# Performance work log

Measured on AMD Instinct MI355X. Metric: run time of the kernel, lower is better.

Reference implementation:

```python
import jax, jax.numpy as jnp
from jax import lax
import numpy as np

L, B, D_IN, D_OUT, D_MLP = 64, 32, 512, 512, 128
WINDOWS = [1, 3]
FEATS = [256, 128]
C = sum(FEATS)  # 384
EPS = 1e-5


def _leaky(x):
    return jnp.where(x >= 0, x, 0.1 * x)


def setup_inputs() -> dict:
    key = jax.random.key(0)
    ks = jax.random.split(key, 16)
    s = lambda k, shp: (jax.random.normal(k, shp, jnp.float32) * 0.02)
    inp = {}
    inp["x"] = jax.random.normal(ks[0], (L, B, D_IN), jnp.float32)
    inp["xs_mask"] = jnp.ones((L, B), jnp.float32)
    # conv + batchnorm params per window
    inp["conv_w0"] = s(ks[1], (FEATS[0], 1, D_IN * WINDOWS[0]))
    inp["conv_b0"] = jnp.zeros((FEATS[0],), jnp.float32)
    inp["gamma0"] = jnp.ones((FEATS[0],), jnp.float32)
    inp["beta0"] = jnp.zeros((FEATS[0],), jnp.float32)
    inp["conv_w1"] = s(ks[2], (FEATS[1], 1, D_IN * WINDOWS[1]))
    inp["conv_b1"] = jnp.zeros((FEATS[1],), jnp.float32)
    inp["gamma1"] = jnp.ones((FEATS[1],), jnp.float32)
    inp["beta1"] = jnp.zeros((FEATS[1],), jnp.float32)
    inp["w0"] = s(ks[3], (2 * C, D_MLP)); inp["b0"] = jnp.zeros((D_MLP,), jnp.float32)
    inp["w1"] = s(ks[4], (D_MLP, D_MLP)); inp["b1"] = jnp.zeros((D_MLP,), jnp.float32)
    inp["w2"] = s(ks[5], (D_MLP, D_MLP)); inp["b2"] = jnp.zeros((D_MLP,), jnp.float32)
    inp["w3"] = s(ks[6], (D_MLP, D_MLP)); inp["b3"] = jnp.zeros((D_MLP,), jnp.float32)
    # output MLP: Linear(d_mlp->d_mlp), Linear(d_mlp->d_out)
    inp["w4"] = s(ks[7], (D_MLP, D_MLP)); inp["b4"] = jnp.zeros((D_MLP,), jnp.float32)
    inp["w5"] = s(ks[8], (D_MLP, D_OUT)); inp["b5"] = jnp.zeros((D_OUT,), jnp.float32)
    return inp


def reference(x, xs_mask, conv_w0, conv_b0, gamma0, beta0, conv_w1, conv_b1,
              gamma1, beta1, w0, b0, w1, b1, w2, b2, w3, b3, w4, b4, w5, b5):
    # x: (L, B, E)
    x = x * xs_mask[:, :, None]
    xf = jnp.transpose(x, (1, 0, 2)).reshape(B, 1, L * D_IN)  # (B, 1, L*E)

    # CNN front-end: Conv1d(stride=d_in) + BatchNorm1d (batch stats) + LeakyReLU
    feats = []
    for win, cw, cb, g, bt in [(WINDOWS[0], conv_w0, conv_b0, gamma0, beta0),
                               (WINDOWS[1], conv_w1, conv_b1, gamma1, beta1)]:
        pad = (win - 1) // 2 * D_IN
        y = lax.conv_general_dilated(xf, cw, window_strides=(D_IN,),
                                     padding=[(pad, pad)],
                                     dimension_numbers=("NCH", "OIH", "NCH"))
        y = y + cb[None, :, None]  # (B, C_k, L)
        m = y.mean(axis=(0, 2))
        v = y.var(axis=(0, 2))  # biased var, as torch BN training mode
        y = (y - m[None, :, None]) / jnp.sqrt(v[None, :, None] + EPS)
        y = y * g[None, :, None] + bt[None, :, None]
        feats.append(_leaky(y))
    h = jnp.concatenate(feats, axis=1)          # (B, C, L)
    h = jnp.transpose(h, (2, 0, 1))             # (L, B, C)
    h = h * xs_mask[:, :, None]

    # Graph propagation: pairwise concat + first linear, split over concat halves
    # cat([h_i, h_j]) @ w0 == h_i @ w0[:C] + h_j @ w0[C:]  (avoids (L,L,B,2C) tensor)
    a = jnp.einsum("lbc,cd->lbd", h, w0[:C])    # (L, B, d_mlp)
    bb = jnp.einsum("lbc,cd->lbd", h, w0[C:])   # (L, B, d_mlp)
    p = _leaky(a[:, None, :, :] + bb[None, :, :, :] + b0)  # (L, L, B, d_mlp)
    p = _leaky(p @ w1 + b1)
    p = _leaky(p @ w2 + b2)
    p = _leaky(p @ w3 + b3)
    p = p * xs_mask[:, None, :, None]
    p = p.mean(axis=1)                          # (L, B, d_mlp)

    out = _leaky(p @ w4 + b4)
    out = _leaky(out @ w5 + b5)                 # (L, B, d_out)
    return out * xs_mask[:, :, None]
```

## Files before the change

### kernel.cpp

```cpp
#include <hip/hip_runtime.h>


#define BB 32
#define CCH 384

__device__ __forceinline__ float leaky(float x) { return fmaxf(x, 0.1f * x); }

typedef _Float16 f16x8 __attribute__((ext_vector_type(8)));
typedef float f32x4 __attribute__((ext_vector_type(4)));

union F8 { uint4 q; f16x8 h; };
union H2 { _Float16 f[2]; uint32_t u; };

__device__ __forceinline__ void split2(float d0, float d1,
                                       uint32_t& hw, uint32_t& lw) {
  H2 h, l;
  h.f[0] = (_Float16)d0; h.f[1] = (_Float16)d1;
  l.f[0] = (_Float16)((d0 - (float)h.f[0]) * 2048.0f);
  l.f[1] = (_Float16)((d1 - (float)h.f[1]) * 2048.0f);
  hw = h.u; lw = l.u;
}

__global__ __launch_bounds__(256) void conv_kernel(
    const float* __restrict__ x, const float* __restrict__ mask,
    const float* __restrict__ cw0, const float* __restrict__ cw1,
    float* __restrict__ yG, float* __restrict__ Ssum, float* __restrict__ Ssq)
{
  __shared__ uint32_t Ah[64 * 68], Al[64 * 68];
  __shared__ uint32_t Bh[64 * 68], Bl[64 * 68];
  int bx = blockIdx.x;
  int nb = bx % 6, mb = bx / 6;
  int n0 = nb * 64;
  int row0 = mb * 64;
  bool w3 = (nb >= 4);
  int nch = w3 ? 12 : 4;
  const float* wbase = w3 ? (cw1 + (n0 - 256) * 1536) : (cw0 + n0 * 512);
  int wK = w3 ? 1536 : 512;

  int tid = threadIdx.x;
  int wid = __builtin_amdgcn_readfirstlane(tid >> 6);
  int wm = wid & 1, wn2 = wid >> 1;
  int lane = tid & 63;
  int m16 = lane & 15, q = lane >> 4;

  f32x4 hi[2][2], cr[2][2];
#pragma unroll
  for (int a = 0; a < 2; ++a)
#pragma unroll
    for (int b = 0; b < 2; ++b) {
      hi[a][b] = (f32x4){0.f, 0.f, 0.f, 0.f};
      cr[a][b] = (f32x4){0.f, 0.f, 0.f, 0.f};
    }

#pragma unroll 1
  for (int ch = 0; ch < nch; ++ch) {
    int kg0 = ch * 128;
    int tap = kg0 >> 9;
    int d0 = kg0 & 511;
    int shift = w3 ? (tap - 1) * 32 : 0;
    __syncthreads();
#pragma unroll 1
    for (int it = 0; it < 4; ++it) {
      int idx = it * 256 + tid;
      int r = idx >> 4;
      int k8 = (idx & 15) * 8;
      float d[8];
      int rowg = row0 + r + shift;
      if ((unsigned)rowg < 2048u) {
        float mv = mask[rowg];
        const float* xp = x + rowg * 512 + d0 + k8;
        float4 a0 = *(const float4*)xp;
        float4 a1 = *(const float4*)(xp + 4);
        d[0] = a0.x * mv; d[1] = a0.y * mv; d[2] = a0.z * mv; d[3] = a0.w * mv;
        d[4] = a1.x * mv; d[5] = a1.y * mv; d[6] = a1.z * mv; d[7] = a1.w * mv;
      } else {
#pragma unroll
        for (int t2 = 0; t2 < 8; ++t2) d[t2] = 0.f;
      }
      uint4 hq, lq;
      split2(d[0], d[1], hq.x, lq.x);
      split2(d[2], d[3], hq.y, lq.y);
      split2(d[4], d[5], hq.z, lq.z);
      split2(d[6], d[7], hq.w, lq.w);
      *(uint4*)&Ah[r * 68 + k8 / 2] = hq;
      *(uint4*)&Al[r * 68 + k8 / 2] = lq;
      const float* wp = wbase + r * wK + kg0 + k8;
      float4 b0v = *(const float4*)wp;
      float4 b1v = *(const float4*)(wp + 4);
      split2(b0v.x, b0v.y, hq.x, lq.x);
      split2(b0v.z, b0v.w, hq.y, lq.y);
      split2(b1v.x, b1v.y, hq.z, lq.z);
      split2(b1v.z, b1v.w, hq.w, lq.w);
      *(uint4*)&Bh[r * 68 + k8 / 2] = hq;
      *(uint4*)&Bl[r * 68 + k8 / 2] = lq;
    }
    __syncthreads();
#pragma unroll
    for (int ks = 0; ks < 4; ++ks) {
      int koff = ks * 16 + q * 4;
      F8 bh[2], bl[2];
#pragma unroll
      for (int nt = 0; nt < 2; ++nt) {
        int br = wn2 * 32 + nt * 16 + m16;
        bh[nt].q = *(const uint4*)&Bh[br * 68 + koff];
        bl[nt].q = *(const uint4*)&Bl[br * 68 + koff];
      }
#pragma unroll
      for (int mt = 0; mt < 2; ++mt) {
        int ar = wm * 32 + mt * 16 + m16;
        F8 ah, al;
        ah.q = *(const uint4*)&Ah[ar * 68 + koff];
        al.q = *(const uint4*)&Al[ar * 68 + koff];
#pragma unroll
        for (int nt = 0; nt < 2; ++nt) {
          hi[mt][nt] = __builtin_amdgcn_mfma_f32_16x16x32_f16(
              ah.h, bh[nt].h, hi[mt][nt], 0, 0, 0);
          cr[mt][nt] = __builtin_amdgcn_mfma_f32_16x16x32_f16(
              ah.h, bl[nt].h, cr[mt][nt], 0, 0, 0);
          cr[mt][nt] = __builtin_amdgcn_mfma_f32_16x16x32_f16(
              al.h, bh[nt].h, cr[mt][nt], 0, 0, 0);
        }
      }
    }
  }

  float y[2][2][4];
#pragma unroll
  for (int mt = 0; mt < 2; ++mt)
#pragma unroll
    for (int nt = 0; nt < 2; ++nt)
#pragma unroll
      for (int rg = 0; rg < 4; ++rg)
        y[mt][nt][rg] = hi[mt][nt][rg] + cr[mt][nt][rg] * (1.0f / 2048.0f);

#pragma unroll
  for (int nt = 0; nt < 2; ++nt) {
    float s = 0.f, s2 = 0.f;
#pragma unroll
    for (int mt = 0; mt < 2; ++mt)
#pragma unroll
      for (int rg = 0; rg < 4; ++rg) {
        float v = y[mt][nt][rg];
        s += v; s2 += v * v;
      }
    s  += __shfl_xor(s, 16, 64);  s  += __shfl_xor(s, 32, 64);
    s2 += __shfl_xor(s2, 16, 64); s2 += __shfl_xor(s2, 32, 64);
    if (lane < 16) {
      int c = n0 + wn2 * 32 + nt * 16 + m16;
      atomicAdd(&Ssum[c], s);
      atomicAdd(&Ssq[c], s2);
    }
  }

  __syncthreads();
  float* Yl = (float*)Ah;
#pragma unroll
  for (int mt = 0; mt < 2; ++mt)
#pragma unroll
    for (int nt = 0; nt < 2; ++nt)
#pragma unroll
      for (int rg = 0; rg < 4; ++rg)
        Yl[(wn2 * 32 + nt * 16 + m16) * 68 + wm * 32 + mt * 16 + q * 4 + rg] =
            y[mt][nt][rg];
  __syncthreads();
  {
    int c = tid >> 2, seg = (tid & 3) * 16;
#pragma unroll
    for (int j = 0; j < 16; j += 4)
      *(float4*)&yG[(n0 + c) * 2048 + row0 + seg + j] =
          *(const float4*)&Yl[c * 68 + seg + j];
  }
}

__global__ __launch_bounds__(256) void ab_kernel(
    const float* __restrict__ yG, const float* __restrict__ Ssum,
    const float* __restrict__ Ssq,
    const float* __restrict__ g0, const float* __restrict__ be0,
    const float* __restrict__ g1, const float* __restrict__ be1,
    const float* __restrict__ mask, const float* __restrict__ w0,
    const float* __restrict__ w1, const float* __restrict__ w2,
    const float* __restrict__ w3, uint32_t* __restrict__ wpk,
    float* __restrict__ a_arr, float* __restrict__ bb_arr)
{
  int bx = blockIdx.x;
  int tid = threadIdx.x;
  if (bx >= 256) {
    int e = (bx - 256) * 256 + tid;
    int L = e >> 13;
    int r = e & 8191;
    int k2 = r >> 7, n = r & 127;
    int k = k2 * 2;
    const float* w = (L == 0) ? w1 : (L == 1) ? w2 : w3;
    uint32_t hw, lw;
    split2(w[k * 128 + n], w[(k + 1) * 128 + n], hw, lw);
    wpk[L * 8192 + n * 64 + k2] = hw;
    wpk[24576 + L * 8192 + n * 64 + k2] = lw;
    return;
  }
  __shared__ float As[32 * 36];
  __shared__ float Ws[32 * 68];
  __shared__ float scs[384], shs[384];
  for (int c = tid; c < 384; c += 256) {
    float Sv = Ssum[c], S2v = Ssq[c];
    float mean = Sv * (1.f / 2048.f);
    float var  = S2v * (1.f / 2048.f) - mean * mean;
    float g  = (c < 256) ? g0[c] : g1[c - 256];
    float be = (c < 256) ? be0[c] : be1[c - 256];
    float sc = g / sqrtf(var + 1e-5f);
    scs[c] = sc;
    shs[c] = be - mean * sc;
  }
  __syncthreads();

  int rt = bx & 63, ct = bx >> 6;
  int row0 = rt * 32, n0 = ct * 64;
  int r4 = (tid >> 5) * 4;
  int n2 = (tid & 31) * 2;
  int scc = tid >> 3, srr4 = (tid & 7) * 4;
  int wnn8 = (tid & 7) * 8;
  const float* wbase = (n0 < 128) ? (w0 + n0) : (w0 + CCH * 128 + (n0 - 128));
  float4 mv = *(const float4*)(mask + row0 + srr4);

  float acc[4][2] = {{0.f, 0.f}};
#pragma unroll 1
  for (int c0 = 0; c0 < 384; c0 += 32) {
    int c = c0 + scc;
    float4 yv = *(const float4*)(yG + c * 2048 + row0 + srr4);
    float sc = scs[c], sh = shs[c];
    float4 wv0 = *(const float4*)(wbase + c * 128 + wnn8);
    float4 wv1 = *(const float4*)(wbase + c * 128 + wnn8 + 4);
    __syncthreads();
    float4 hv;
    hv.x = leaky(fmaf(yv.x, sc, sh)) * mv.x;
    hv.y = leaky(fmaf(yv.y, sc, sh)) * mv.y;
    hv.z = leaky(fmaf(yv.z, sc, sh)) * mv.z;
    hv.w = leaky(fmaf(yv.w, sc, sh)) * mv.w;
    *(float4*)&As[scc * 36 + srr4] = hv;
    *(float4*)&Ws[scc * 68 + wnn8] = wv0;
    *(float4*)&Ws[scc * 68 + wnn8 + 4] = wv1;
    __syncthreads();
#pragma unroll
    for (int cc = 0; cc < 32; ++cc) {
      float4 a = *(const float4*)&As[cc * 36 + r4];
      float2 w = *(const float2*)&Ws[cc * 68 + n2];
      acc[0][0] = fmaf(a.x, w.x, acc[0][0]); acc[0][1] = fmaf(a.x, w.y, acc[0][1]);
      acc[1][0] = fmaf(a.y, w.x, acc[1][0]); acc[1][1] = fmaf(a.y, w.y, acc[1][1]);
      acc[2][0] = fmaf(a.z, w.x, acc[2][0]); acc[2][1] = fmaf(a.z, w.y, acc[2][1]);
      acc[3][0] = fmaf(a.w, w.x, acc[3][0]); acc[3][1] = fmaf(a.w, w.y, acc[3][1]);
    }
  }
  float* dst; int nd;
  if (n0 < 128) { dst = a_arr; nd = n0; } else { dst = bb_arr; nd = n0 - 128; }
#pragma unroll
  for (int ri = 0; ri < 4; ++ri)
    *(float2*)&dst[(row0 + r4 + ri) * 128 + nd + n2] = make_float2(acc[ri][0], acc[ri][1]);
}

__global__ __launch_bounds__(512, 3) void pair_kernel(
    const float* __restrict__ a_arr, const float* __restrict__ bb_arr,
    const float* __restrict__ b0, const uint32_t* __restrict__ wpk,
    const float* __restrict__ b1, const float* __restrict__ b2,
    const float* __restrict__ b3,
    const float* __restrict__ w4, const float* __restrict__ b4,
    const float* __restrict__ w5, const float* __restrict__ b5,
    const float* __restrict__ mask, float* __restrict__ out)
{
  __shared__ uint32_t Ahs[64 * 68];
  __shared__ uint32_t Als[64 * 68];
  int i = blockIdx.x, b = blockIdx.y;
  int tid = threadIdx.x;
  int browp = i * BB + b;

  int wid = __builtin_amdgcn_readfirstlane(tid >> 6);
  int lane = tid & 63;
  int m16 = lane & 15, q = lane >> 4;
  int wn16 = wid * 16;
  int wrow = wn16 + m16;

  F8 Wh, Wl, Whn, Wln;
  {
    const uint32_t* W0h = wpk + wrow * 64 + q * 4;
    const uint32_t* W0l = wpk + 24576 + wrow * 64 + q * 4;
    Wh.q = *(const uint4*)W0h;
    Wl.q = *(const uint4*)W0l;
  }

  {
    int k8 = (tid & 15) * 8;
    const float* ap = a_arr + browp * 128 + k8;
    const float* zp = b0 + k8;
    float az[8];
#pragma unroll
    for (int t = 0; t < 8; t += 4) {
      float4 av = *(const float4*)(ap + t);
      float4 zv = *(const float4*)(zp + t);
      az[t + 0] = av.x + zv.x; az[t + 1] = av.y + zv.y;
      az[t + 2] = av.z + zv.z; az[t + 3] = av.w + zv.w;
    }
#pragma unroll
    for (int it = 0; it < 2; ++it) {
      int r = (it * 512 + tid) >> 4;
      const float* bbp = bb_arr + (r * BB + b) * 128 + k8;
      float d[8];
#pragma unroll
      for (int t = 0; t < 8; t += 4) {
        float4 bv = *(const float4*)(bbp + t);
        d[t + 0] = leaky(az[t + 0] + bv.x);
        d[t + 1] = leaky(az[t + 1] + bv.y);
        d[t + 2] = leaky(az[t + 2] + bv.z);
        d[t + 3] = leaky(az[t + 3] + bv.w);
      }
      uint4 hq, lq;
      split2(d[0], d[1], hq.x, lq.x);
      split2(d[2], d[3], hq.y, lq.y);
      split2(d[4], d[5], hq.z, lq.z);
      split2(d[6], d[7], hq.w, lq.w);
      *(uint4*)&Ahs[r * 68 + k8 / 2] = hq;
      *(uint4*)&Als[r * 68 + k8 / 2] = lq;
    }
  }
  __syncthreads();

  f32x4 hi[4], cr[4];

#pragma unroll 1
  for (int L = 0; L < 3; ++L) {
    const uint32_t* WhL = wpk + L * 8192;
    const uint32_t* WlL = wpk + 24576 + L * 8192;
    const float* Bv = (L == 0) ? b1 : (L == 1) ? b2 : b3;
#pragma unroll
    for (int mt = 0; mt < 4; ++mt) {
      hi[mt] = (f32x4){0.f, 0.f, 0.f, 0.f};
      cr[mt] = (f32x4){0.f, 0.f, 0.f, 0.f};
    }

#pragma unroll
    for (int ks = 0; ks < 4; ++ks) {
      int koff = ks * 16 + q * 4;
      if (ks < 3) {
        Whn.q = *(const uint4*)(WhL + wrow * 64 + koff + 16);
        Wln.q = *(const uint4*)(WlL + wrow * 64 + koff + 16);
      } else if (L < 2) {
        Whn.q = *(const uint4*)(WhL + 8192 + wrow * 64 + q * 4);
        Wln.q = *(const uint4*)(WlL + 8192 + wrow * 64 + q * 4);
      }
#pragma unroll
      for (int mt = 0; mt < 4; ++mt) {
        int arow = mt * 16 + m16;
        F8 Ah, Al;
        Ah.q = *(const uint4*)&Ahs[arow * 68 + koff];
        Al.q = *(const uint4*)&Als[arow * 68 + koff];
        hi[mt] = __builtin_amdgcn_mfma_f32_16x16x32_f16(
            Ah.h, Wh.h, hi[mt], 0, 0, 0);
        cr[mt] = __builtin_amdgcn_mfma_f32_16x16x32_f16(
            Ah.h, Wl.h, cr[mt], 0, 0, 0);
        cr[mt] = __builtin_amdgcn_mfma_f32_16x16x32_f16(
            Al.h, Wh.h, cr[mt], 0, 0, 0);
      }
      Wh = Whn; Wl = Wln;
    }

    float bias = Bv[wrow];

    if (L < 2) {
      __syncthreads();
      int par = lane & 1;
      int colw = (wn16 + (m16 & ~1)) >> 1;
#pragma unroll
      for (int mt = 0; mt < 4; ++mt) {
#pragma unroll
        for (int rg = 0; rg < 4; ++rg) {
          float d = leaky(hi[mt][rg] + cr[mt][rg] * (1.0f / 2048.0f) + bias);
          float dn = __shfl_xor(d, 1, 64);
          float de = par ? dn : d;
          float do_ = par ? d : dn;
          uint32_t hw, lw;
          split2(de, do_, hw, lw);
          int row = mt * 16 + q * 4 + rg;
          if (par) Als[row * 68 + colw] = lw;
          else     Ahs[row * 68 + colw] = hw;
        }
      }
      __syncthreads();
    } else {
      float s = 0.f;
#pragma unroll
      for (int mt = 0; mt < 4; ++mt)
#pragma unroll
        for (int rg = 0; rg < 4; ++rg)
          s += leaky(hi[mt][rg] + cr[mt][rg] * (1.0f / 2048.0f) + bias);
      s += __shfl_xor(s, 16, 64);
      s += __shfl_xor(s, 32, 64);
      float mfac = (1.0f / 64.0f) * mask[browp];
      __syncthreads();
      float* scratch = (float*)Ahs;
      float* Pm = scratch;
      float* Tp = scratch + 128;
      float* T4 = scratch + 640;
      if (lane < 16) Pm[wrow] = s * mfac;
      __syncthreads();
      {
        int k = tid & 127, chh = tid >> 7;
        const float* w4c = w4 + (chh * 32) * 128 + k;
        const float* pc = Pm + chh * 32;
        float t = 0.f;
#pragma unroll 8
        for (int c0 = 0; c0 < 32; c0 += 4) {
          float4 pv = *(const float4*)&pc[c0];
          t = fmaf(pv.x, w4c[(c0 + 0) * 128], t);
          t = fmaf(pv.y, w4c[(c0 + 1) * 128], t);
          t = fmaf(pv.z, w4c[(c0 + 2) * 128], t);
          t = fmaf(pv.w, w4c[(c0 + 3) * 128], t);
        }
        Tp[chh * 128 + k] = t;
      }
      __syncthreads();
      if (tid < 128)
        T4[tid] = leaky(Tp[tid] + Tp[128 + tid] + Tp[256 + tid] +
                        Tp[384 + tid] + b4[tid]);
      __syncthreads();
      {
        float o = b5[tid];
#pragma unroll 4
        for (int c0 = 0; c0 < 128; c0 += 4) {
          float4 tv = *(const float4*)&T4[c0];
          o = fmaf(tv.x, w5[(c0 + 0) * 512 + tid], o);
          o = fmaf(tv.y, w5[(c0 + 1) * 512 + tid], o);
          o = fmaf(tv.z, w5[(c0 + 2) * 512 + tid], o);
          o = fmaf(tv.w, w5[(c0 + 3) * 512 + tid], o);
        }
        out[browp * 512 + tid] = leaky(o) * mask[browp];
      }
    }
  }
}

extern "C" void kernel_launch(void* const* d_in, const int* in_sizes, int n_in,
                              void* d_out, int out_size, void* d_ws, size_t ws_size,
                              hipStream_t stream) {
  const float* x    = (const float*)d_in[0];
  const float* mask = (const float*)d_in[1];
  const float* cw0  = (const float*)d_in[2];
  const float* g0   = (const float*)d_in[4];
  const float* be0  = (const float*)d_in[5];
  const float* cw1  = (const float*)d_in[6];
  const float* g1   = (const float*)d_in[8];
  const float* be1  = (const float*)d_in[9];
  const float* w0   = (const float*)d_in[10];
  const float* b0   = (const float*)d_in[11];
  const float* w1   = (const float*)d_in[12];
  const float* b1   = (const float*)d_in[13];
  const float* w2   = (const float*)d_in[14];
  const float* b2   = (const float*)d_in[15];
  const float* w3   = (const float*)d_in[16];
  const float* b3   = (const float*)d_in[17];
  const float* w4   = (const float*)d_in[18];
  const float* b4   = (const float*)d_in[19];
  const float* w5   = (const float*)d_in[20];
  const float* b5   = (const float*)d_in[21];

  float* ws     = (float*)d_ws;
  float* Ssum   = ws;
  float* Ssq    = ws + 384;
  float* yG     = ws + 768;
  uint32_t* wpk = (uint32_t*)(ws + 787200);
  float* a_arr  = ws + 836352;
  float* bb_arr = ws + 1098496;
  float* outp   = (float*)d_out;

  hipMemsetAsync(Ssum, 0, 768 * sizeof(float), stream);
  conv_kernel<<<192, 256, 0, stream>>>(x, mask, cw0, cw1, yG, Ssum, Ssq);
  ab_kernel<<<352, 256, 0, stream>>>(yG, Ssum, Ssq, g0, be0, g1, be1,
                                     mask, w0, w1, w2, w3, wpk, a_arr, bb_arr);
  dim3 g5(64, 32);
  pair_kernel<<<g5, 512, 0, stream>>>(a_arr, bb_arr, b0, wpk, b1, b2, b3,
                                      w4, b4, w5, b5, mask, outp);
}
```

Baseline: 267.8 us.

## Rebalance conv and projection kernels across more blocks, move weight packing

```diff
diff --git a/kernel.cpp b/kernel.cpp
--- a/kernel.cpp
+++ b/kernel.cpp
@@ -24,163 +24,10 @@
 __global__ __launch_bounds__(256) void conv_kernel(
     const float* __restrict__ x, const float* __restrict__ mask,
     const float* __restrict__ cw0, const float* __restrict__ cw1,
-    float* __restrict__ yG, float* __restrict__ Ssum, float* __restrict__ Ssq)
-{
-  __shared__ uint32_t Ah[64 * 68], Al[64 * 68];
-  __shared__ uint32_t Bh[64 * 68], Bl[64 * 68];
-  int bx = blockIdx.x;
-  int nb = bx % 6, mb = bx / 6;
-  int n0 = nb * 64;
-  int row0 = mb * 64;
-  bool w3 = (nb >= 4);
-  int nch = w3 ? 12 : 4;
-  const float* wbase = w3 ? (cw1 + (n0 - 256) * 1536) : (cw0 + n0 * 512);
-  int wK = w3 ? 1536 : 512;
-
-  int tid = threadIdx.x;
-  int wid = __builtin_amdgcn_readfirstlane(tid >> 6);
-  int wm = wid & 1, wn2 = wid >> 1;
-  int lane = tid & 63;
-  int m16 = lane & 15, q = lane >> 4;
-
-  f32x4 hi[2][2], cr[2][2];
-#pragma unroll
-  for (int a = 0; a < 2; ++a)
-#pragma unroll
-    for (int b = 0; b < 2; ++b) {
-      hi[a][b] = (f32x4){0.f, 0.f, 0.f, 0.f};
-      cr[a][b] = (f32x4){0.f, 0.f, 0.f, 0.f};
-    }
-
-#pragma unroll 1
-  for (int ch = 0; ch < nch; ++ch) {
-    int kg0 = ch * 128;
-    int tap = kg0 >> 9;
-    int d0 = kg0 & 511;
-    int shift = w3 ? (tap - 1) * 32 : 0;
-    __syncthreads();
-#pragma unroll 1
-    for (int it = 0; it < 4; ++it) {
-      int idx = it * 256 + tid;
-      int r = idx >> 4;
-      int k8 = (idx & 15) * 8;
-      float d[8];
-      int rowg = row0 + r + shift;
-      if ((unsigned)rowg < 2048u) {
-        float mv = mask[rowg];
-        const float* xp = x + rowg * 512 + d0 + k8;
-        float4 a0 = *(const float4*)xp;
-        float4 a1 = *(const float4*)(xp + 4);
-        d[0] = a0.x * mv; d[1] = a0.y * mv; d[2] = a0.z * mv; d[3] = a0.w * mv;
-        d[4] = a1.x * mv; d[5] = a1.y * mv; d[6] = a1.z * mv; d[7] = a1.w * mv;
-      } else {
-#pragma unroll
-        for (int t2 = 0; t2 < 8; ++t2) d[t2] = 0.f;
-      }
-      uint4 hq, lq;
-      split2(d[0], d[1], hq.x, lq.x);
-      split2(d[2], d[3], hq.y, lq.y);
-      split2(d[4], d[5], hq.z, lq.z);
-      split2(d[6], d[7], hq.w, lq.w);
-      *(uint4*)&Ah[r * 68 + k8 / 2] = hq;
-      *(uint4*)&Al[r * 68 + k8 / 2] = lq;
-      const float* wp = wbase + r * wK + kg0 + k8;
-      float4 b0v = *(const float4*)wp;
-      float4 b1v = *(const float4*)(wp + 4);
-      split2(b0v.x, b0v.y, hq.x, lq.x);
-      split2(b0v.z, b0v.w, hq.y, lq.y);
-      split2(b1v.x, b1v.y, hq.z, lq.z);
-      split2(b1v.z, b1v.w, hq.w, lq.w);
-      *(uint4*)&Bh[r * 68 + k8 / 2] = hq;
-      *(uint4*)&Bl[r * 68 + k8 / 2] = lq;
-    }
-    __syncthreads();
-#pragma unroll
-    for (int ks = 0; ks < 4; ++ks) {
-      int koff = ks * 16 + q * 4;
-      F8 bh[2], bl[2];
-#pragma unroll
-      for (int nt = 0; nt < 2; ++nt) {
-        int br = wn2 * 32 + nt * 16 + m16;
-        bh[nt].q = *(const uint4*)&Bh[br * 68 + koff];
-        bl[nt].q = *(const uint4*)&Bl[br * 68 + koff];
-      }
-#pragma unroll
-      for (int mt = 0; mt < 2; ++mt) {
-        int ar = wm * 32 + mt * 16 + m16;
-        F8 ah, al;
-        ah.q = *(const uint4*)&Ah[ar * 68 + koff];
-        al.q = *(const uint4*)&Al[ar * 68 + koff];
-#pragma unroll
-        for (int nt = 0; nt < 2; ++nt) {
-          hi[mt][nt] = __builtin_amdgcn_mfma_f32_16x16x32_f16(
-              ah.h, bh[nt].h, hi[mt][nt], 0, 0, 0);
-          cr[mt][nt] = __builtin_amdgcn_mfma_f32_16x16x32_f16(
-              ah.h, bl[nt].h, cr[mt][nt], 0, 0, 0);
-          cr[mt][nt] = __builtin_amdgcn_mfma_f32_16x16x32_f16(
-              al.h, bh[nt].h, cr[mt][nt], 0, 0, 0);
-        }
-      }
-    }
-  }
-
-  float y[2][2][4];
-#pragma unroll
-  for (int mt = 0; mt < 2; ++mt)
-#pragma unroll
-    for (int nt = 0; nt < 2; ++nt)
-#pragma unroll
-      for (int rg = 0; rg < 4; ++rg)
-        y[mt][nt][rg] = hi[mt][nt][rg] + cr[mt][nt][rg] * (1.0f / 2048.0f);
-
-#pragma unroll
-  for (int nt = 0; nt < 2; ++nt) {
-    float s = 0.f, s2 = 0.f;
-#pragma unroll
-    for (int mt = 0; mt < 2; ++mt)
-#pragma unroll
-      for (int rg = 0; rg < 4; ++rg) {
-        float v = y[mt][nt][rg];
-        s += v; s2 += v * v;
-      }
-    s  += __shfl_xor(s, 16, 64);  s  += __shfl_xor(s, 32, 64);
-    s2 += __shfl_xor(s2, 16, 64); s2 += __shfl_xor(s2, 32, 64);
-    if (lane < 16) {
-      int c = n0 + wn2 * 32 + nt * 16 + m16;
-      atomicAdd(&Ssum[c], s);
-      atomicAdd(&Ssq[c], s2);
-    }
-  }
-
-  __syncthreads();
-  float* Yl = (float*)Ah;
-#pragma unroll
-  for (int mt = 0; mt < 2; ++mt)
-#pragma unroll
-    for (int nt = 0; nt < 2; ++nt)
-#pragma unroll
-      for (int rg = 0; rg < 4; ++rg)
-        Yl[(wn2 * 32 + nt * 16 + m16) * 68 + wm * 32 + mt * 16 + q * 4 + rg] =
-            y[mt][nt][rg];
-  __syncthreads();
-  {
-    int c = tid >> 2, seg = (tid & 3) * 16;
-#pragma unroll
-    for (int j = 0; j < 16; j += 4)
-      *(float4*)&yG[(n0 + c) * 2048 + row0 + seg + j] =
-          *(const float4*)&Yl[c * 68 + seg + j];
-  }
-}
-
-__global__ __launch_bounds__(256) void ab_kernel(
-    const float* __restrict__ yG, const float* __restrict__ Ssum,
-    const float* __restrict__ Ssq,
-    const float* __restrict__ g0, const float* __restrict__ be0,
-    const float* __restrict__ g1, const float* __restrict__ be1,
-    const float* __restrict__ mask, const float* __restrict__ w0,
     const float* __restrict__ w1, const float* __restrict__ w2,
-    const float* __restrict__ w3, uint32_t* __restrict__ wpk,
-    float* __restrict__ a_arr, float* __restrict__ bb_arr)
+    const float* __restrict__ w3,
+    float* __restrict__ yG, float* __restrict__ Ssum, float* __restrict__ Ssq,
+    uint32_t* __restrict__ wpk)
 {
   int bx = blockIdx.x;
   int tid = threadIdx.x;
@@ -197,8 +44,287 @@
     wpk[24576 + L * 8192 + n * 64 + k2] = lw;
     return;
   }
-  __shared__ float As[32 * 36];
-  __shared__ float Ws[32 * 68];
+
+  __shared__ uint32_t Ah[64 * 68], Al[64 * 68];
+  __shared__ uint32_t Bh[64 * 68], Bl[64 * 68];
+
+  int wid = __builtin_amdgcn_readfirstlane(tid >> 6);
+  int lane = tid & 63;
+  int m16 = lane & 15, q = lane >> 4;
+
+  if (bx < 128) {
+    int nb = bx & 3, mb = bx >> 2;
+    int n0 = nb * 64;
+    int row0 = mb * 64;
+    const float* wbase = cw0 + n0 * 512;
+    int wm = wid & 1, wn2 = wid >> 1;
+
+    f32x4 hi[2][2], cr[2][2];
+#pragma unroll
+    for (int a = 0; a < 2; ++a)
+#pragma unroll
+      for (int b = 0; b < 2; ++b) {
+        hi[a][b] = (f32x4){0.f, 0.f, 0.f, 0.f};
+        cr[a][b] = (f32x4){0.f, 0.f, 0.f, 0.f};
+      }
+
+#pragma unroll 1
+    for (int ch = 0; ch < 4; ++ch) {
+      int kg0 = ch * 128;
+      __syncthreads();
+#pragma unroll 1
+      for (int it = 0; it < 4; ++it) {
+        int idx = it * 256 + tid;
+        int r = idx >> 4;
+        int k8 = (idx & 15) * 8;
+        float d[8];
+        int rowg = row0 + r;
+        {
+          float mv = mask[rowg];
+          const float* xp = x + rowg * 512 + kg0 + k8;
+          float4 a0 = *(const float4*)xp;
+          float4 a1 = *(const float4*)(xp + 4);
+          d[0] = a0.x * mv; d[1] = a0.y * mv; d[2] = a0.z * mv; d[3] = a0.w * mv;
+          d[4] = a1.x * mv; d[5] = a1.y * mv; d[6] = a1.z * mv; d[7] = a1.w * mv;
+        }
+        uint4 hq, lq;
+        split2(d[0], d[1], hq.x, lq.x);
+        split2(d[2], d[3], hq.y, lq.y);
+        split2(d[4], d[5], hq.z, lq.z);
+        split2(d[6], d[7], hq.w, lq.w);
+        *(uint4*)&Ah[r * 68 + k8 / 2] = hq;
+        *(uint4*)&Al[r * 68 + k8 / 2] = lq;
+        const float* wp = wbase + r * 512 + kg0 + k8;
+        float4 b0v = *(const float4*)wp;
+        float4 b1v = *(const float4*)(wp + 4);
+        split2(b0v.x, b0v.y, hq.x, lq.x);
+        split2(b0v.z, b0v.w, hq.y, lq.y);
+        split2(b1v.x, b1v.y, hq.z, lq.z);
+        split2(b1v.z, b1v.w, hq.w, lq.w);
+        *(uint4*)&Bh[r * 68 + k8 / 2] = hq;
+        *(uint4*)&Bl[r * 68 + k8 / 2] = lq;
+      }
+      __syncthreads();
+#pragma unroll
+      for (int ks = 0; ks < 4; ++ks) {
+        int koff = ks * 16 + q * 4;
+        F8 bh[2], bl[2];
+#pragma unroll
+        for (int nt = 0; nt < 2; ++nt) {
+          int br = wn2 * 32 + nt * 16 + m16;
+          bh[nt].q = *(const uint4*)&Bh[br * 68 + koff];
+          bl[nt].q = *(const uint4*)&Bl[br * 68 + koff];
+        }
+#pragma unroll
+        for (int mt = 0; mt < 2; ++mt) {
+          int ar = wm * 32 + mt * 16 + m16;
+          F8 ah, al;
+          ah.q = *(const uint4*)&Ah[ar * 68 + koff];
+          al.q = *(const uint4*)&Al[ar * 68 + koff];
+#pragma unroll
+          for (int nt = 0; nt < 2; ++nt) {
+            hi[mt][nt] = __builtin_amdgcn_mfma_f32_16x16x32_f16(
+                ah.h, bh[nt].h, hi[mt][nt], 0, 0, 0);
+            cr[mt][nt] = __builtin_amdgcn_mfma_f32_16x16x32_f16(
+                ah.h, bl[nt].h, cr[mt][nt], 0, 0, 0);
+            cr[mt][nt] = __builtin_amdgcn_mfma_f32_16x16x32_f16(
+                al.h, bh[nt].h, cr[mt][nt], 0, 0, 0);
+          }
+        }
+      }
+    }
+
+    float y[2][2][4];
+#pragma unroll
+    for (int mt = 0; mt < 2; ++mt)
+#pragma unroll
+      for (int nt = 0; nt < 2; ++nt)
+#pragma unroll
+        for (int rg = 0; rg < 4; ++rg)
+          y[mt][nt][rg] = hi[mt][nt][rg] + cr[mt][nt][rg] * (1.0f / 2048.0f);
+
+#pragma unroll
+    for (int nt = 0; nt < 2; ++nt) {
+      float s = 0.f, s2 = 0.f;
+#pragma unroll
+      for (int mt = 0; mt < 2; ++mt)
+#pragma unroll
+        for (int rg = 0; rg < 4; ++rg) {
+          float v = y[mt][nt][rg];
+          s += v; s2 += v * v;
+        }
+      s  += __shfl_xor(s, 16, 64);  s  += __shfl_xor(s, 32, 64);
+      s2 += __shfl_xor(s2, 16, 64); s2 += __shfl_xor(s2, 32, 64);
+      if (lane < 16) {
+        int c = n0 + wn2 * 32 + nt * 16 + m16;
+        atomicAdd(&Ssum[c], s);
+        atomicAdd(&Ssq[c], s2);
+      }
+    }
+
+    __syncthreads();
+    float* Yl = (float*)Ah;
+#pragma unroll
+    for (int mt = 0; mt < 2; ++mt)
+#pragma unroll
+      for (int nt = 0; nt < 2; ++nt)
+#pragma unroll
+        for (int rg = 0; rg < 4; ++rg)
+          Yl[(wn2 * 32 + nt * 16 + m16) * 68 + wm * 32 + mt * 16 + q * 4 + rg] =
+              y[mt][nt][rg];
+    __syncthreads();
+    {
+      int c = tid >> 2, seg = (tid & 3) * 16;
+#pragma unroll
+      for (int j = 0; j < 16; j += 4)
+        *(float4*)&yG[(n0 + c) * 2048 + row0 + seg + j] =
+            *(const float4*)&Yl[c * 68 + seg + j];
+    }
+    return;
+  }
+
+  {
+    int t = bx - 128;
+    int nb3 = t & 1, mb3 = t >> 1;
+    int n0 = 256 + nb3 * 64;
+    int row0 = mb3 * 32;
+    const float* wbase = cw1 + (n0 - 256) * 1536;
+
+    f32x4 hi3[2], cr3[2];
+#pragma unroll
+    for (int mt = 0; mt < 2; ++mt) {
+      hi3[mt] = (f32x4){0.f, 0.f, 0.f, 0.f};
+      cr3[mt] = (f32x4){0.f, 0.f, 0.f, 0.f};
+    }
+
+#pragma unroll 1
+    for (int ch = 0; ch < 12; ++ch) {
+      int kg0 = ch * 128;
+      int tap = kg0 >> 9;
+      int d0 = kg0 & 511;
+      int shift = (tap - 1) * 32;
+      __syncthreads();
+#pragma unroll 1
+      for (int it = 0; it < 6; ++it) {
+        int idx = it * 256 + tid;
+        if (idx < 512) {
+          int r = idx >> 4;
+          int k8 = (idx & 15) * 8;
+          float d[8];
+          int rowg = row0 + r + shift;
+          if ((unsigned)rowg < 2048u) {
+            float mv = mask[rowg];
+            const float* xp = x + rowg * 512 + d0 + k8;
+            float4 a0 = *(const float4*)xp;
+            float4 a1 = *(const float4*)(xp + 4);
+            d[0] = a0.x * mv; d[1] = a0.y * mv; d[2] = a0.z * mv; d[3] = a0.w * mv;
+            d[4] = a1.x * mv; d[5] = a1.y * mv; d[6] = a1.z * mv; d[7] = a1.w * mv;
+          } else {
+#pragma unroll
+            for (int t2 = 0; t2 < 8; ++t2) d[t2] = 0.f;
+          }
+          uint4 hq, lq;
+          split2(d[0], d[1], hq.x, lq.x);
+          split2(d[2], d[3], hq.y, lq.y);
+          split2(d[4], d[5], hq.z, lq.z);
+          split2(d[6], d[7], hq.w, lq.w);
+          *(uint4*)&Ah[r * 68 + k8 / 2] = hq;
+          *(uint4*)&Al[r * 68 + k8 / 2] = lq;
+        } else {
+          int idx2 = idx - 512;
+          int r = idx2 >> 4;
+          int k8 = (idx2 & 15) * 8;
+          const float* wp = wbase + r * 1536 + kg0 + k8;
+          float4 b0v = *(const float4*)wp;
+          float4 b1v = *(const float4*)(wp + 4);
+          uint4 hq, lq;
+          split2(b0v.x, b0v.y, hq.x, lq.x);
+          split2(b0v.z, b0v.w, hq.y, lq.y);
+          split2(b1v.x, b1v.y, hq.z, lq.z);
+          split2(b1v.z, b1v.w, hq.w, lq.w);
+          *(uint4*)&Bh[r * 68 + k8 / 2] = hq;
+          *(uint4*)&Bl[r * 68 + k8 / 2] = lq;
+        }
+      }
+      __syncthreads();
+#pragma unroll
+      for (int ks = 0; ks < 4; ++ks) {
+        int koff = ks * 16 + q * 4;
+        F8 bh, bl;
+        int br = wid * 16 + m16;
+        bh.q = *(const uint4*)&Bh[br * 68 + koff];
+        bl.q = *(const uint4*)&Bl[br * 68 + koff];
+#pragma unroll
+        for (int mt = 0; mt < 2; ++mt) {
+          int ar = mt * 16 + m16;
+          F8 ah, al;
+          ah.q = *(const uint4*)&Ah[ar * 68 + koff];
+          al.q = *(const uint4*)&Al[ar * 68 + koff];
+          hi3[mt] = __builtin_amdgcn_mfma_f32_16x16x32_f16(
+              ah.h, bh.h, hi3[mt], 0, 0, 0);
+          cr3[mt] = __builtin_amdgcn_mfma_f32_16x16x32_f16(
+              ah.h, bl.h, cr3[mt], 0, 0, 0);
+          cr3[mt] = __builtin_amdgcn_mfma_f32_16x16x32_f16(
+              al.h, bh.h, cr3[mt], 0, 0, 0);
+        }
+      }
+    }
+
+    float y3[2][4];
+#pragma unroll
+    for (int mt = 0; mt < 2; ++mt)
+#pragma unroll
+      for (int rg = 0; rg < 4; ++rg)
+        y3[mt][rg] = hi3[mt][rg] + cr3[mt][rg] * (1.0f / 2048.0f);
+
+    {
+      float s = 0.f, s2 = 0.f;
+#pragma unroll
+      for (int mt = 0; mt < 2; ++mt)
+#pragma unroll
+        for (int rg = 0; rg < 4; ++rg) {
+          float v = y3[mt][rg];
+          s += v; s2 += v * v;
+        }
+      s  += __shfl_xor(s, 16, 64);  s  += __shfl_xor(s, 32, 64);
+      s2 += __shfl_xor(s2, 16, 64); s2 += __shfl_xor(s2, 32, 64);
+      if (lane < 16) {
+        int c = n0 + wid * 16 + m16;
+        atomicAdd(&Ssum[c], s);
+        atomicAdd(&Ssq[c], s2);
+      }
+    }
+
+    __syncthreads();
+    float* Yl = (float*)Ah;
+#pragma unroll
+    for (int mt = 0; mt < 2; ++mt)
+#pragma unroll
+      for (int rg = 0; rg < 4; ++rg)
+        Yl[(wid * 16 + m16) * 34 + mt * 16 + q * 4 + rg] = y3[mt][rg];
+    __syncthreads();
+    {
+      int c = tid >> 2, seg = (tid & 3) * 8;
+#pragma unroll
+      for (int j = 0; j < 8; j += 4)
+        *(float4*)&yG[(n0 + c) * 2048 + row0 + seg + j] =
+            *(const float4*)&Yl[c * 34 + seg + j];
+    }
+  }
+}
+
+__global__ __launch_bounds__(256) void ab_kernel(
+    const float* __restrict__ yG, const float* __restrict__ Ssum,
+    const float* __restrict__ Ssq,
+    const float* __restrict__ g0, const float* __restrict__ be0,
+    const float* __restrict__ g1, const float* __restrict__ be1,
+    const float* __restrict__ mask, const float* __restrict__ w0,
+    float* __restrict__ a_arr, float* __restrict__ bb_arr)
+{
+  int bx = blockIdx.x;
+  int tid = threadIdx.x;
+  __shared__ float As[64 * 20];
+  __shared__ float Ws[64 * 68];
   __shared__ float scs[384], shs[384];
   for (int c = tid; c < 384; c += 256) {
     float Sv = Ssum[c], S2v = Ssq[c];
@@ -212,48 +338,53 @@
   }
   __syncthreads();
 
-  int rt = bx & 63, ct = bx >> 6;
-  int row0 = rt * 32, n0 = ct * 64;
-  int r4 = (tid >> 5) * 4;
-  int n2 = (tid & 31) * 2;
-  int scc = tid >> 3, srr4 = (tid & 7) * 4;
-  int wnn8 = (tid & 7) * 8;
+  int rt = bx >> 2, ct = bx & 3;
+  int row0 = rt * 16, n0 = ct * 64;
+  int cth = tid >> 2;
+  int srr4 = (tid & 3) * 4;
+  int wn16 = (tid & 3) * 16;
+  int r4 = (tid >> 6) * 4;
+  int n1 = tid & 63;
   const float* wbase = (n0 < 128) ? (w0 + n0) : (w0 + CCH * 128 + (n0 - 128));
   float4 mv = *(const float4*)(mask + row0 + srr4);
 
-  float acc[4][2] = {{0.f, 0.f}};
+  float acc[4] = {0.f, 0.f, 0.f, 0.f};
 #pragma unroll 1
-  for (int c0 = 0; c0 < 384; c0 += 32) {
-    int c = c0 + scc;
+  for (int c0 = 0; c0 < 384; c0 += 64) {
+    int c = c0 + cth;
     float4 yv = *(const float4*)(yG + c * 2048 + row0 + srr4);
     float sc = scs[c], sh = shs[c];
-    float4 wv0 = *(const float4*)(wbase + c * 128 + wnn8);
-    float4 wv1 = *(const float4*)(wbase + c * 128 + wnn8 + 4);
+    float4 wv0 = *(const float4*)(wbase + c * 128 + wn16);
+    float4 wv1 = *(const float4*)(wbase + c * 128 + wn16 + 4);
+    float4 wv2 = *(const float4*)(wbase + c * 128 + wn16 + 8);
+    float4 wv3 = *(const float4*)(wbase + c * 128 + wn16 + 12);
     __syncthreads();
     float4 hv;
     hv.x = leaky(fmaf(yv.x, sc, sh)) * mv.x;
     hv.y = leaky(fmaf(yv.y, sc, sh)) * mv.y;
     hv.z = leaky(fmaf(yv.z, sc, sh)) * mv.z;
     hv.w = leaky(fmaf(yv.w, sc, sh)) * mv.w;
-    *(float4*)&As[scc * 36 + srr4] = hv;
-    *(float4*)&Ws[scc * 68 + wnn8] = wv0;
-    *(float4*)&Ws[scc * 68 + wnn8 + 4] = wv1;
+    *(float4*)&As[cth * 20 + srr4] = hv;
+    *(float4*)&Ws[cth * 68 + wn16]      = wv0;
+    *(float4*)&Ws[cth * 68 + wn16 + 4]  = wv1;
+    *(float4*)&Ws[cth * 68 + wn16 + 8]  = wv2;
+    *(float4*)&Ws[cth * 68 + wn16 + 12] = wv3;
     __syncthreads();
-#pragma unroll
-    for (int cc = 0; cc < 32; ++cc) {
-      float4 a = *(const float4*)&As[cc * 36 + r4];
-      float2 w = *(const float2*)&Ws[cc * 68 + n2];
-      acc[0][0] = fmaf(a.x, w.x, acc[0][0]); acc[0][1] = fmaf(a.x, w.y, acc[0][1]);
-      acc[1][0] = fmaf(a.y, w.x, acc[1][0]); acc[1][1] = fmaf(a.y, w.y, acc[1][1]);
-      acc[2][0] = fmaf(a.z, w.x, acc[2][0]); acc[2][1] = fmaf(a.z, w.y, acc[2][1]);
-      acc[3][0] = fmaf(a.w, w.x, acc[3][0]); acc[3][1] = fmaf(a.w, w.y, acc[3][1]);
+#pragma unroll 16
+    for (int cc = 0; cc < 64; ++cc) {
+      float4 a = *(const float4*)&As[cc * 20 + r4];
+      float w  = Ws[cc * 68 + n1];
+      acc[0] = fmaf(a.x, w, acc[0]);
+      acc[1] = fmaf(a.y, w, acc[1]);
+      acc[2] = fmaf(a.z, w, acc[2]);
+      acc[3] = fmaf(a.w, w, acc[3]);
     }
   }
   float* dst; int nd;
   if (n0 < 128) { dst = a_arr; nd = n0; } else { dst = bb_arr; nd = n0 - 128; }
 #pragma unroll
   for (int ri = 0; ri < 4; ++ri)
-    *(float2*)&dst[(row0 + r4 + ri) * 128 + nd + n2] = make_float2(acc[ri][0], acc[ri][1]);
+    dst[(row0 + r4 + ri) * 128 + nd + n1] = acc[ri];
 }
 
 __global__ __launch_bounds__(512, 3) void pair_kernel(
@@ -469,9 +600,10 @@
   float* outp   = (float*)d_out;
 
   hipMemsetAsync(Ssum, 0, 768 * sizeof(float), stream);
-  conv_kernel<<<192, 256, 0, stream>>>(x, mask, cw0, cw1, yG, Ssum, Ssq);
-  ab_kernel<<<352, 256, 0, stream>>>(yG, Ssum, Ssq, g0, be0, g1, be1,
-                                     mask, w0, w1, w2, w3, wpk, a_arr, bb_arr);
+  conv_kernel<<<352, 256, 0, stream>>>(x, mask, cw0, cw1, w1, w2, w3,
+                                       yG, Ssum, Ssq, wpk);
+  ab_kernel<<<512, 256, 0, stream>>>(yG, Ssum, Ssq, g0, be0, g1, be1,
+                                     mask, w0, a_arr, bb_arr);
   dim3 g5(64, 32);
   pair_kernel<<<g5, 512, 0, stream>>>(a_arr, bb_arr, b0, wpk, b1, b2, b3,
                                       w4, b4, w5, b5, mask, outp);
```

New measurement: 269.0 us. About the same (+0.4%).
